# Performance work log

Hardware: AMD Instinct MI355X
Metric: run time of the kernel (lower is better)

## Reference

```python
import math
import jax, jax.numpy as jnp
import numpy as np
from jax import lax

N, L = 256, 4096
DIM_LINEAR, DIM_CONV, KERNEL, STRIDE = 64, 128, 15, 1


def setup_inputs() -> dict:
    key = jax.random.key(0)
    ks = jax.random.split(key, 10)
    tokens = jax.random.randint(ks[0], (N, L), 0, 4, dtype=jnp.int32)
    emb = jax.random.normal(ks[1], (4, DIM_LINEAR), dtype=jnp.float32)
    conv_w = jax.random.normal(ks[2], (DIM_CONV, DIM_LINEAR, KERNEL), dtype=jnp.float32) * (1.0 / math.sqrt(DIM_LINEAR * KERNEL))
    conv_b = jax.random.normal(ks[3], (DIM_CONV,), dtype=jnp.float32) * 0.01
    s = 1.0 / math.sqrt(DIM_CONV)
    Wq = jax.random.normal(ks[4], (DIM_CONV, DIM_CONV), dtype=jnp.float32) * s
    bq = jax.random.normal(ks[5], (DIM_CONV,), dtype=jnp.float32) * 0.01
    Wk = jax.random.normal(ks[6], (DIM_CONV, DIM_CONV), dtype=jnp.float32) * s
    bk = jax.random.normal(ks[7], (DIM_CONV,), dtype=jnp.float32) * 0.01
    Wv = jax.random.normal(ks[8], (DIM_CONV, DIM_CONV), dtype=jnp.float32) * s
    bv = jax.random.normal(ks[9], (DIM_CONV,), dtype=jnp.float32) * 0.01
    return {"tokens": tokens, "emb": emb, "conv_w": conv_w, "conv_b": conv_b,
            "Wq": Wq, "bq": bq, "Wk": Wk, "bk": bk, "Wv": Wv, "bv": bv}


def reference(tokens, emb, conv_w, conv_b, Wq, bq, Wk, bk, Wv, bv):
    # embedding: [N, L, dl] -> channels-first [N, dl, L]
    x = emb[tokens].transpose(0, 2, 1)
    # conv1d, valid padding: [N, dc, Lout]
    y = lax.conv_general_dilated(x, conv_w, window_strides=(STRIDE,),
                                 padding='VALID',
                                 dimension_numbers=('NCH', 'OIH', 'NCH'))
    y = y + conv_b[None, :, None]
    read = y.transpose(0, 2, 1)                      # [N, Lout, dc]
    read_mean = read.mean(axis=1)                    # [N, dc]
    q = read_mean @ Wq.T + bq                        # [N, dc]
    k = read @ Wk.T + bk                             # [N, Lout, dc]
    v = read @ Wv.T + bv                             # [N, Lout, dc]
    scores = jnp.einsum('nd,nld->nl', q, k) / math.sqrt(DIM_CONV)
    attn = jax.nn.softmax(scores, axis=1)            # [N, Lout]
    out = jnp.einsum('nl,nld->nd', attn, v)          # [N, dc]
    return out
```

## Files before the change

### kernel.cpp

```cpp
#include <hip/hip_runtime.h>
#include <math.h>

#define NN 256
#define LL 4096
#define DL 64
#define DC 128
#define KS 15
#define LOUT (LL - KS + 1)
#define RSQRT_DC 0.08838834764831843f
#define INV_LOUT (1.0f / (float)LOUT)

#define WS_CTB  0
#define WS_PACK 7680
#define WS_CNT  73216

__global__ __launch_bounds__(256) void prep_kernel(const int* __restrict__ tokens,
                                                   const float* __restrict__ emb,
                                                   const float* __restrict__ conv_w,
                                                   float* __restrict__ ws) {
    const int b = blockIdx.x, tid = threadIdx.x;
    if (b < NN) {
        __shared__ int totw[4][4];
        const int n = b;
        const int4* tv = (const int4*)(tokens + (size_t)n * LL) + tid * 4;
        unsigned w = 0;
#pragma unroll
        for (int m = 0; m < 4; ++m) {
            int4 t4 = tv[m];
            w |= ((unsigned)t4.x | ((unsigned)t4.y << 2) |
                  ((unsigned)t4.z << 4) | ((unsigned)t4.w << 6)) << (8 * m);
        }
        ((unsigned*)ws)[WS_PACK + n * 256 + tid] = w;
        int c0, c1, c2, c3;
        unsigned y, z;
        y = w;               z = (y | (y >> 1)) & 0x55555555u; c0 = 16 - __popc(z);
        y = w ^ 0x55555555u; z = (y | (y >> 1)) & 0x55555555u; c1 = 16 - __popc(z);
        y = w ^ 0xAAAAAAAAu; z = (y | (y >> 1)) & 0x55555555u; c2 = 16 - __popc(z);
        y = w ^ 0xFFFFFFFFu; z = (y | (y >> 1)) & 0x55555555u; c3 = 16 - __popc(z);
#pragma unroll
        for (int off = 32; off > 0; off >>= 1) {
            c0 += __shfl_down(c0, off, 64); c1 += __shfl_down(c1, off, 64);
            c2 += __shfl_down(c2, off, 64); c3 += __shfl_down(c3, off, 64);
        }
        if ((tid & 63) == 0) {
            const int wv = tid >> 6;
            totw[wv][0] = c0; totw[wv][1] = c1; totw[wv][2] = c2; totw[wv][3] = c3;
        }
        __syncthreads();
        if (tid < 4)
            ((int*)ws)[WS_CNT + n * 4 + tid] =
                totw[0][tid] + totw[1][tid] + totw[2][tid] + totw[3][tid];
    } else {
        const int c = b - NN;
        __shared__ float wsm[DL][16];
        __shared__ float es[4][DL];
        const float* wsrc = conv_w + (size_t)c * (DL * KS);
        for (int idx = tid; idx < DL * KS; idx += 256) wsm[idx / KS][idx % KS] = wsrc[idx];
        es[tid >> 6][tid & 63] = emb[tid];
        __syncthreads();
        if (tid < 60) {
            const int v = tid / KS, k = tid % KS;
            float s = 0.f;
#pragma unroll
            for (int i = 0; i < DL; ++i) s += es[v][i] * wsm[i][k];
            ws[WS_CTB + tid * DC + c] = s;
        }
    }
}

template <int NW>
__device__ __forceinline__ float bsum(float v, float* red, int tid) {
#pragma unroll
    for (int off = 32; off > 0; off >>= 1) v += __shfl_down(v, off, 64);
    if ((tid & 63) == 0) red[tid >> 6] = v;
    __syncthreads();
    float r = 0.f;
#pragma unroll
    for (int w = 0; w < NW; ++w) r += red[w];
    __syncthreads();
    return r;
}

template <int NW>
__device__ __forceinline__ float bmax(float v, float* red, int tid) {
#pragma unroll
    for (int off = 32; off > 0; off >>= 1) v = fmaxf(v, __shfl_down(v, off, 64));
    if ((tid & 63) == 0) red[tid >> 6] = v;
    __syncthreads();
    float r = red[0];
#pragma unroll
    for (int w = 1; w < NW; ++w) r = fmaxf(r, red[w]);
    __syncthreads();
    return r;
}

__global__ __launch_bounds__(512) void encode_kernel(
    const float* __restrict__ ws, const float* __restrict__ conv_b,
    const float* __restrict__ Wq, const float* __restrict__ bq,
    const float* __restrict__ Wk, const float* __restrict__ bk,
    const float* __restrict__ Wv, const float* __restrict__ bv,
    float* __restrict__ out) {
    const int n = blockIdx.x, tid = threadIdx.x;
    const float* ctb = ws + WS_CTB;
    const unsigned* packed = (const unsigned*)ws + WS_PACK;

    __shared__ unsigned tok2L[258];
    __shared__ float stabL[64];
    __shared__ float cfL[60];
    __shared__ float rmL[DC], qvL[DC], qkL[DC], zvL[DC];
    __shared__ float Tt[1024];
    __shared__ float AccL[45];
    __shared__ float red[8];

    if (tid >= 64) {
        const int i = tid - 64;
        if (i < 258) tok2L[i] = (i < 256) ? packed[n * 256 + i] : 0u;
        else if (i < 258 + 45) AccL[i - 258] = 0.f;
    } else {
        const int l = tid;
        const int4 ct = *(const int4*)((const int*)ws + WS_CNT + n * 4);
        const unsigned dwF = packed[n * 256];
        const unsigned dwL = packed[n * 256 + 255];
        if (l < KS) {
            const int k = l;
            const unsigned pm = (k == 0) ? 0u : ((1u << (2 * k)) - 1u);
            const unsigned sm = (k == 14) ? 0u : (0xFFFFFFFFu << (2 * (k + 2)));
            const int tot4[4] = {ct.x, ct.y, ct.z, ct.w};
#pragma unroll
            for (int v = 0; v < 4; ++v) {
                const unsigned patt = (unsigned)v * 0x55555555u;
                unsigned yf = dwF ^ patt, zf = (yf | (yf >> 1)) & 0x55555555u;
                unsigned yl = dwL ^ patt, zl = (yl | (yl >> 1)) & 0x55555555u;
                const int pre = k - __popc(zf & pm);
                const int suf = (14 - k) - __popc(zl & sm);
                cfL[v * KS + k] = (float)(tot4[v] - pre - suf);
            }
        }
        const int c0 = 2 * l, c1 = 2 * l + 1;
        float r0 = 0.f, r1 = 0.f;
        for (int j = 0; j < 60; ++j) {
            const float cfj = cfL[j];
            const float2 cb = *(const float2*)(ctb + j * DC + c0);
            r0 += cfj * cb.x; r1 += cfj * cb.y;
        }
        const float2 cb2 = *(const float2*)(conv_b + c0);
        r0 = cb2.x + r0 * INV_LOUT; r1 = cb2.y + r1 * INV_LOUT;
        rmL[c0] = r0; rmL[c1] = r1;
        const float4* wq0 = (const float4*)(Wq + (size_t)c0 * DC);
        const float4* wq1 = (const float4*)(Wq + (size_t)c1 * DC);
        const float4* rr = (const float4*)rmL;
        float s0 = 0.f, s1 = 0.f;
#pragma unroll 8
        for (int j = 0; j < 32; ++j) {
            const float4 r = rr[j], a = wq0[j], b = wq1[j];
            s0 += a.x * r.x + a.y * r.y + a.z * r.z + a.w * r.w;
            s1 += b.x * r.x + b.y * r.y + b.z * r.z + b.w * r.w;
        }
        const float2 bq2 = *(const float2*)(bq + c0);
        const float qv0 = s0 + bq2.x, qv1 = s1 + bq2.y;
        qvL[c0] = qv0; qvL[c1] = qv1;
        float k0 = 0.f, k1 = 0.f;
        const float4* qq = (const float4*)qvL;
        for (int c4 = 0; c4 < 32; ++c4) {
            const float4 q4 = qq[c4];
            const float2 w0 = *(const float2*)(Wk + (size_t)(4 * c4 + 0) * DC + c0);
            const float2 w1 = *(const float2*)(Wk + (size_t)(4 * c4 + 1) * DC + c0);
            const float2 w2 = *(const float2*)(Wk + (size_t)(4 * c4 + 2) * DC + c0);
            const float2 w3 = *(const float2*)(Wk + (size_t)(4 * c4 + 3) * DC + c0);
            k0 += q4.x * w0.x + q4.y * w1.x + q4.z * w2.x + q4.w * w3.x;
            k1 += q4.x * w0.y + q4.y * w1.y + q4.z * w2.y + q4.w * w3.y;
        }
        qkL[c0] = k0; qkL[c1] = k1;
        if (l < 60) {
            const float4* cr = (const float4*)(ctb + (size_t)l * DC);
            const float4* qk4 = (const float4*)qkL;
            float s = 0.f;
#pragma unroll 8
            for (int t = 0; t < 32; ++t) {
                const float4 a = cr[t], q = qk4[t];
                s += a.x * q.x + a.y * q.y + a.z * q.z + a.w * q.w;
            }
            stabL[l] = s * RSQRT_DC;
        }
        const float2 bk2 = *(const float2*)(bk + c0);
        float t = cb2.x * k0 + cb2.y * k1 + qv0 * bk2.x + qv1 * bk2.y;
#pragma unroll
        for (int off = 32; off > 0; off >>= 1) t += __shfl_down(t, off, 64);
        if (l == 0) stabL[60] = t * RSQRT_DC;
    }
    __syncthreads();

    const float base = stabL[60];
    for (int e = tid; e < 1024; e += 512) {
        const int j = e >> 8, bb = e & 255;
        float s = stabL[(bb & 3) * KS + 4 * j] +
                  stabL[((bb >> 2) & 3) * KS + 4 * j + 1] +
                  stabL[((bb >> 4) & 3) * KS + 4 * j + 2];
        if (j < 3) s += stabL[((bb >> 6) & 3) * KS + 4 * j + 3];
        Tt[e] = s;
    }
    __syncthreads();

    const unsigned d0 = tok2L[tid >> 1], d1 = tok2L[(tid >> 1) + 1];
    const unsigned long long W = (unsigned long long)d0 | ((unsigned long long)d1 << 32);
    const int sbase = (tid & 1) << 4;
    const int t0 = tid * 8;
    float sc[8];
    float lmax = -3.4e38f;
#pragma unroll
    for (int p = 0; p < 8; ++p) {
        const unsigned w = (unsigned)(W >> (sbase + 2 * p));
        const float s = base + Tt[w & 255] + Tt[256 + ((w >> 8) & 255)] +
                        Tt[512 + ((w >> 16) & 255)] + Tt[768 + ((w >> 24) & 63)];
        sc[p] = (t0 + p < LOUT) ? s : -3.4e38f;
        lmax = fmaxf(lmax, sc[p]);
    }
    const float m = bmax<8>(lmax, red, tid);
    float lsum = 0.f;
#pragma unroll
    for (int p = 0; p < 8; ++p) {
        const float e = (t0 + p < LOUT) ? __expf(sc[p] - m) : 0.f;
        sc[p] = e; lsum += e;
    }
    const float S = bsum<8>(lsum, red, tid);
    const float invS = 1.0f / S;

    float a1[KS], a2[KS], a3[KS];
#pragma unroll
    for (int k = 0; k < KS; ++k) { a1[k] = 0.f; a2[k] = 0.f; a3[k] = 0.f; }
#pragma unroll
    for (int p = 0; p < 8; ++p) {
        const float e = sc[p];
        const unsigned w = (unsigned)(W >> (sbase + 2 * p));
#pragma unroll
        for (int k = 0; k < KS; ++k) {
            const int v = (int)((w >> (2 * k)) & 3u);
            a1[k] += (v == 1) ? e : 0.f;
            a2[k] += (v == 2) ? e : 0.f;
            a3[k] += (v == 3) ? e : 0.f;
        }
    }
    {
        const int lane = tid & 63;
#pragma unroll
        for (int k = 0; k < KS; ++k) {
            float v1 = a1[k], v2 = a2[k], v3 = a3[k];
#pragma unroll
            for (int off = 32; off > 0; off >>= 1) {
                v1 += __shfl_down(v1, off, 64);
                v2 += __shfl_down(v2, off, 64);
                v3 += __shfl_down(v3, off, 64);
            }
            if (lane == 0) {
                atomicAdd(&AccL[k], v1);
                atomicAdd(&AccL[KS + k], v2);
                atomicAdd(&AccL[2 * KS + k], v3);
            }
        }
    }
    __syncthreads();

    if (tid < DC) {
        float s = 0.f;
#pragma unroll
        for (int k = 0; k < KS; ++k) {
            const float a0 = S - AccL[k] - AccL[KS + k] - AccL[2 * KS + k];
            s += a0 * ctb[k * DC + tid];
        }
#pragma unroll
        for (int j = KS; j < 60; ++j) s += AccL[j - KS] * ctb[j * DC + tid];
        zvL[tid] = conv_b[tid] + s * invS;
    }
    __syncthreads();

    if (tid < DC) {
        const float4* wr = (const float4*)(Wv + (size_t)tid * DC);
        const float4* z4 = (const float4*)zvL;
        float s = 0.f;
#pragma unroll 8
        for (int j = 0; j < 32; ++j) {
            const float4 w = wr[j], z = z4[j];
            s += w.x * z.x + w.y * z.y + w.z * z.z + w.w * z.w;
        }
        out[(size_t)n * DC + tid] = s + bv[tid];
    }
}

extern "C" void kernel_launch(void* const* d_in, const int* in_sizes, int n_in,
                              void* d_out, int out_size, void* d_ws, size_t ws_size,
                              hipStream_t stream) {
    const int*   tokens = (const int*)d_in[0];
    const float* emb    = (const float*)d_in[1];
    const float* conv_w = (const float*)d_in[2];
    const float* conv_b = (const float*)d_in[3];
    const float* Wq     = (const float*)d_in[4];
    const float* bq     = (const float*)d_in[5];
    const float* Wk     = (const float*)d_in[6];
    const float* bk     = (const float*)d_in[7];
    const float* Wv     = (const float*)d_in[8];
    const float* bv     = (const float*)d_in[9];
    float* out = (float*)d_out;
    float* ws  = (float*)d_ws;

    prep_kernel<<<NN + DC, 256, 0, stream>>>(tokens, emb, conv_w, ws);
    encode_kernel<<<NN, 512, 0, stream>>>(ws, conv_b, Wq, bq, Wk, bk, Wv, bv, out);
}
```

Before: 100.5 us.

## Precompute weight-projected conv tables and replace max reduction with analytic bound

Adds a small prep2 kernel that folds Wq, Wk and Wv into the 60-row conv token table once per call: projected Q/K/V tables plus bias scalars. Each per-sample encode block then needs only short dot products instead of three 128x128 matvecs. The softmax block-max reduction is replaced by an upper bound built from per-position table maxima, which removes one block reduction and its barriers. The cost is a third kernel launch with a serial dependency. The bound may also sit well above the true max, raising underflow risk in exp.

```diff
diff --git a/kernel.cpp b/kernel.cpp
--- a/kernel.cpp
+++ b/kernel.cpp
@@ -10,14 +10,21 @@
 #define RSQRT_DC 0.08838834764831843f
 #define INV_LOUT (1.0f / (float)LOUT)
 
-#define WS_CTB  0
-#define WS_PACK 7680
-#define WS_CNT  73216
-
-__global__ __launch_bounds__(256) void prep_kernel(const int* __restrict__ tokens,
-                                                   const float* __restrict__ emb,
-                                                   const float* __restrict__ conv_w,
-                                                   float* __restrict__ ws) {
+#define WS_CTB   0
+#define WS_QC    7680
+#define WS_KC    15360
+#define WS_G     23040
+#define WS_S0    30720
+#define WS_BB    30784
+#define WS_B0    30848
+#define WS_OUTB  30976
+#define WS_PACK  31104
+#define WS_CNT   96640
+
+__global__ __launch_bounds__(256) void prep1_kernel(const int* __restrict__ tokens,
+                                                    const float* __restrict__ emb,
+                                                    const float* __restrict__ conv_w,
+                                                    float* __restrict__ ws) {
     const int b = blockIdx.x, tid = threadIdx.x;
     if (b < NN) {
         __shared__ int totw[4][4];
@@ -68,46 +75,100 @@
     }
 }
 
-template <int NW>
-__device__ __forceinline__ float bsum(float v, float* red, int tid) {
-#pragma unroll
-    for (int off = 32; off > 0; off >>= 1) v += __shfl_down(v, off, 64);
-    if ((tid & 63) == 0) red[tid >> 6] = v;
-    __syncthreads();
-    float r = 0.f;
-#pragma unroll
-    for (int w = 0; w < NW; ++w) r += red[w];
-    __syncthreads();
-    return r;
-}
-
-template <int NW>
-__device__ __forceinline__ float bmax(float v, float* red, int tid) {
-#pragma unroll
-    for (int off = 32; off > 0; off >>= 1) v = fmaxf(v, __shfl_down(v, off, 64));
-    if ((tid & 63) == 0) red[tid >> 6] = v;
-    __syncthreads();
-    float r = red[0];
-#pragma unroll
-    for (int w = 1; w < NW; ++w) r = fmaxf(r, red[w]);
-    __syncthreads();
-    return r;
-}
-
-__global__ __launch_bounds__(512) void encode_kernel(
-    const float* __restrict__ ws, const float* __restrict__ conv_b,
+__global__ __launch_bounds__(128) void prep2_kernel(
+    const float* __restrict__ conv_b,
     const float* __restrict__ Wq, const float* __restrict__ bq,
     const float* __restrict__ Wk, const float* __restrict__ bk,
     const float* __restrict__ Wv, const float* __restrict__ bv,
-    float* __restrict__ out) {
+    float* __restrict__ ws) {
+    const int j = blockIdx.x, c = threadIdx.x;
+    __shared__ float cbL[DC];
+    __shared__ float red2a[2], red2b[2];
+    cbL[c] = conv_b[c];
+    if (j < 60) {
+        __shared__ float ctbj[DC];
+        ctbj[c] = ws[WS_CTB + j * DC + c];
+        __syncthreads();
+        const float4* wq = (const float4*)(Wq + (size_t)c * DC);
+        const float4* wk = (const float4*)(Wk + (size_t)c * DC);
+        const float4* wv = (const float4*)(Wv + (size_t)c * DC);
+        const float4* ct4 = (const float4*)ctbj;
+        const float4* cb4 = (const float4*)cbL;
+        float qc = 0.f, q0c = 0.f, kc = 0.f, kcbc = 0.f, gc = 0.f;
+#pragma unroll 8
+        for (int t = 0; t < 32; ++t) {
+            const float4 a = wq[t], b = wk[t], g = wv[t], x = ct4[t], y = cb4[t];
+            qc   += a.x * x.x + a.y * x.y + a.z * x.z + a.w * x.w;
+            q0c  += a.x * y.x + a.y * y.y + a.z * y.z + a.w * y.w;
+            kc   += b.x * x.x + b.y * x.y + b.z * x.z + b.w * x.w;
+            kcbc += b.x * y.x + b.y * y.y + b.z * y.z + b.w * y.w;
+            gc   += g.x * x.x + g.y * x.y + g.z * x.z + g.w * x.w;
+        }
+        ws[WS_QC + j * DC + c] = qc;
+        ws[WS_KC + j * DC + c] = kc;
+        ws[WS_G  + j * DC + c] = gc;
+        const float beta = kcbc + bk[c];
+        q0c += bq[c];
+        float t1 = kc * q0c;
+        float t2 = qc * beta;
+#pragma unroll
+        for (int off = 32; off > 0; off >>= 1) {
+            t1 += __shfl_down(t1, off, 64);
+            t2 += __shfl_down(t2, off, 64);
+        }
+        if ((c & 63) == 0) { red2a[c >> 6] = t1; red2b[c >> 6] = t2; }
+        __syncthreads();
+        if (c == 0) {
+            ws[WS_S0 + j] = (red2a[0] + red2a[1]) * RSQRT_DC;
+            ws[WS_BB + j] = (red2b[0] + red2b[1]) * RSQRT_DC;
+        }
+    } else {
+        __syncthreads();
+        const float4* wq = (const float4*)(Wq + (size_t)c * DC);
+        const float4* wk = (const float4*)(Wk + (size_t)c * DC);
+        const float4* wv = (const float4*)(Wv + (size_t)c * DC);
+        const float4* cb4 = (const float4*)cbL;
+        float q0c = 0.f, kcbc = 0.f, ob = 0.f;
+#pragma unroll 8
+        for (int t = 0; t < 32; ++t) {
+            const float4 a = wq[t], b = wk[t], g = wv[t], y = cb4[t];
+            q0c  += a.x * y.x + a.y * y.y + a.z * y.z + a.w * y.w;
+            kcbc += b.x * y.x + b.y * y.y + b.z * y.z + b.w * y.w;
+            ob   += g.x * y.x + g.y * y.y + g.z * y.z + g.w * y.w;
+        }
+        ws[WS_OUTB + c] = ob + bv[c];
+        q0c += bq[c];
+        float t1 = q0c * (kcbc + bk[c]);
+#pragma unroll
+        for (int off = 32; off > 0; off >>= 1) t1 += __shfl_down(t1, off, 64);
+        if ((c & 63) == 0) red2a[c >> 6] = t1;
+        __syncthreads();
+        if (c == 0) ws[WS_B0] = (red2a[0] + red2a[1]) * RSQRT_DC;
+    }
+}
+
+template <int NW>
+__device__ __forceinline__ float bsum(float v, float* red, int tid) {
+#pragma unroll
+    for (int off = 32; off > 0; off >>= 1) v += __shfl_down(v, off, 64);
+    if ((tid & 63) == 0) red[tid >> 6] = v;
+    __syncthreads();
+    float r = 0.f;
+#pragma unroll
+    for (int w = 0; w < NW; ++w) r += red[w];
+    __syncthreads();
+    return r;
+}
+
+__global__ __launch_bounds__(512) void encode_kernel(
+    const float* __restrict__ ws, float* __restrict__ out) {
     const int n = blockIdx.x, tid = threadIdx.x;
-    const float* ctb = ws + WS_CTB;
     const unsigned* packed = (const unsigned*)ws + WS_PACK;
 
     __shared__ unsigned tok2L[258];
     __shared__ float stabL[64];
     __shared__ float cfL[60];
-    __shared__ float rmL[DC], qvL[DC], qkL[DC], zvL[DC];
+    __shared__ float uL[DC];
     __shared__ float Tt[1024];
     __shared__ float AccL[45];
     __shared__ float red[8];
@@ -133,60 +194,32 @@
                 unsigned yl = dwL ^ patt, zl = (yl | (yl >> 1)) & 0x55555555u;
                 const int pre = k - __popc(zf & pm);
                 const int suf = (14 - k) - __popc(zl & sm);
-                cfL[v * KS + k] = (float)(tot4[v] - pre - suf);
+                cfL[v * KS + k] = (float)(tot4[v] - pre - suf) * INV_LOUT;
             }
         }
-        const int c0 = 2 * l, c1 = 2 * l + 1;
-        float r0 = 0.f, r1 = 0.f;
+        const int c0 = 2 * l;
+        float u0 = 0.f, u1 = 0.f;
         for (int j = 0; j < 60; ++j) {
             const float cfj = cfL[j];
-            const float2 cb = *(const float2*)(ctb + j * DC + c0);
-            r0 += cfj * cb.x; r1 += cfj * cb.y;
-        }
-        const float2 cb2 = *(const float2*)(conv_b + c0);
-        r0 = cb2.x + r0 * INV_LOUT; r1 = cb2.y + r1 * INV_LOUT;
-        rmL[c0] = r0; rmL[c1] = r1;
-        const float4* wq0 = (const float4*)(Wq + (size_t)c0 * DC);
-        const float4* wq1 = (const float4*)(Wq + (size_t)c1 * DC);
-        const float4* rr = (const float4*)rmL;
-        float s0 = 0.f, s1 = 0.f;
-#pragma unroll 8
-        for (int j = 0; j < 32; ++j) {
-            const float4 r = rr[j], a = wq0[j], b = wq1[j];
-            s0 += a.x * r.x + a.y * r.y + a.z * r.z + a.w * r.w;
-            s1 += b.x * r.x + b.y * r.y + b.z * r.z + b.w * r.w;
-        }
-        const float2 bq2 = *(const float2*)(bq + c0);
-        const float qv0 = s0 + bq2.x, qv1 = s1 + bq2.y;
-        qvL[c0] = qv0; qvL[c1] = qv1;
-        float k0 = 0.f, k1 = 0.f;
-        const float4* qq = (const float4*)qvL;
-        for (int c4 = 0; c4 < 32; ++c4) {
-            const float4 q4 = qq[c4];
-            const float2 w0 = *(const float2*)(Wk + (size_t)(4 * c4 + 0) * DC + c0);
-            const float2 w1 = *(const float2*)(Wk + (size_t)(4 * c4 + 1) * DC + c0);
-            const float2 w2 = *(const float2*)(Wk + (size_t)(4 * c4 + 2) * DC + c0);
-            const float2 w3 = *(const float2*)(Wk + (size_t)(4 * c4 + 3) * DC + c0);
-            k0 += q4.x * w0.x + q4.y * w1.x + q4.z * w2.x + q4.w * w3.x;
-            k1 += q4.x * w0.y + q4.y * w1.y + q4.z * w2.y + q4.w * w3.y;
-        }
-        qkL[c0] = k0; qkL[c1] = k1;
+            const float2 q2 = *(const float2*)(ws + WS_QC + j * DC + c0);
+            u0 += cfj * q2.x; u1 += cfj * q2.y;
+        }
+        uL[c0] = u0; uL[c0 + 1] = u1;
+        float t = (l < 60) ? cfL[l] * ws[WS_BB + l] : 0.f;
+#pragma unroll
+        for (int off = 32; off > 0; off >>= 1) t += __shfl_down(t, off, 64);
+        if (l == 0) stabL[60] = ws[WS_B0] + t;
         if (l < 60) {
-            const float4* cr = (const float4*)(ctb + (size_t)l * DC);
-            const float4* qk4 = (const float4*)qkL;
+            const float4* kr = (const float4*)(ws + WS_KC + (size_t)l * DC);
+            const float4* u4 = (const float4*)uL;
             float s = 0.f;
 #pragma unroll 8
-            for (int t = 0; t < 32; ++t) {
-                const float4 a = cr[t], q = qk4[t];
-                s += a.x * q.x + a.y * q.y + a.z * q.z + a.w * q.w;
+            for (int t2 = 0; t2 < 32; ++t2) {
+                const float4 a = kr[t2], u = u4[t2];
+                s += a.x * u.x + a.y * u.y + a.z * u.z + a.w * u.w;
             }
-            stabL[l] = s * RSQRT_DC;
-        }
-        const float2 bk2 = *(const float2*)(bk + c0);
-        float t = cb2.x * k0 + cb2.y * k1 + qv0 * bk2.x + qv1 * bk2.y;
-#pragma unroll
-        for (int off = 32; off > 0; off >>= 1) t += __shfl_down(t, off, 64);
-        if (l == 0) stabL[60] = t * RSQRT_DC;
+            stabL[l] = ws[WS_S0 + l] + s * RSQRT_DC;
+        }
     }
     __syncthreads();
 
@@ -199,28 +232,26 @@
         if (j < 3) s += stabL[((bb >> 6) & 3) * KS + 4 * j + 3];
         Tt[e] = s;
     }
+    float M = base;
+#pragma unroll
+    for (int k = 0; k < KS; ++k)
+        M += fmaxf(fmaxf(stabL[k], stabL[KS + k]),
+                   fmaxf(stabL[2 * KS + k], stabL[3 * KS + k]));
     __syncthreads();
 
     const unsigned d0 = tok2L[tid >> 1], d1 = tok2L[(tid >> 1) + 1];
     const unsigned long long W = (unsigned long long)d0 | ((unsigned long long)d1 << 32);
     const int sbase = (tid & 1) << 4;
     const int t0 = tid * 8;
-    float sc[8];
-    float lmax = -3.4e38f;
+    float ev[8];
+    float lsum = 0.f;
 #pragma unroll
     for (int p = 0; p < 8; ++p) {
         const unsigned w = (unsigned)(W >> (sbase + 2 * p));
         const float s = base + Tt[w & 255] + Tt[256 + ((w >> 8) & 255)] +
                         Tt[512 + ((w >> 16) & 255)] + Tt[768 + ((w >> 24) & 63)];
-        sc[p] = (t0 + p < LOUT) ? s : -3.4e38f;
-        lmax = fmaxf(lmax, sc[p]);
-    }
-    const float m = bmax<8>(lmax, red, tid);
-    float lsum = 0.f;
-#pragma unroll
-    for (int p = 0; p < 8; ++p) {
-        const float e = (t0 + p < LOUT) ? __expf(sc[p] - m) : 0.f;
-        sc[p] = e; lsum += e;
+        const float e = (t0 + p < LOUT) ? __expf(s - M) : 0.f;
+        ev[p] = e; lsum += e;
     }
     const float S = bsum<8>(lsum, red, tid);
     const float invS = 1.0f / S;
@@ -230,7 +261,7 @@
     for (int k = 0; k < KS; ++k) { a1[k] = 0.f; a2[k] = 0.f; a3[k] = 0.f; }
 #pragma unroll
     for (int p = 0; p < 8; ++p) {
-        const float e = sc[p];
+        const float e = ev[p];
         const unsigned w = (unsigned)(W >> (sbase + 2 * p));
 #pragma unroll
         for (int k = 0; k < KS; ++k) {
@@ -265,24 +296,11 @@
 #pragma unroll
         for (int k = 0; k < KS; ++k) {
             const float a0 = S - AccL[k] - AccL[KS + k] - AccL[2 * KS + k];
-            s += a0 * ctb[k * DC + tid];
-        }
-#pragma unroll
-        for (int j = KS; j < 60; ++j) s += AccL[j - KS] * ctb[j * DC + tid];
-        zvL[tid] = conv_b[tid] + s * invS;
-    }
-    __syncthreads();
-
-    if (tid < DC) {
-        const float4* wr = (const float4*)(Wv + (size_t)tid * DC);
-        const float4* z4 = (const float4*)zvL;
-        float s = 0.f;
-#pragma unroll 8
-        for (int j = 0; j < 32; ++j) {
-            const float4 w = wr[j], z = z4[j];
-            s += w.x * z.x + w.y * z.y + w.z * z.z + w.w * z.w;
-        }
-        out[(size_t)n * DC + tid] = s + bv[tid];
+            s += a0 * ws[WS_G + k * DC + tid];
+        }
+#pragma unroll
+        for (int j = KS; j < 60; ++j) s += AccL[j - KS] * ws[WS_G + j * DC + tid];
+        out[(size_t)n * DC + tid] = ws[WS_OUTB + tid] + s * invS;
     }
 }
 
@@ -302,6 +320,7 @@
     float* out = (float*)d_out;
     float* ws  = (float*)d_ws;
 
-    prep_kernel<<<NN + DC, 256, 0, stream>>>(tokens, emb, conv_w, ws);
-    encode_kernel<<<NN, 512, 0, stream>>>(ws, conv_b, Wq, bq, Wk, bk, Wv, bv, out);
-}
+    prep1_kernel<<<NN + DC, 256, 0, stream>>>(tokens, emb, conv_w, ws);
+    prep2_kernel<<<61, 128, 0, stream>>>(conv_b, Wq, bq, Wk, bk, Wv, bv, ws);
+    encode_kernel<<<NN, 512, 0, stream>>>(ws, out);
+}
```

After: 104.8 us. 1.04x slower.
